# Performance work log

Hardware: AMD Instinct MI355X
Metric: run time of the kernel (lower is better)

The kernel has to match this reference:

```python
import jax, jax.numpy as jnp
import numpy as np

EPS = 1e-6
NUM_HEADS = 16

def layernorm(x, alpha, bias):
    # Faithful to the torch module: torch.std uses ddof=1, and eps is added to std.
    mean = jnp.mean(x, axis=-1, keepdims=True)
    std = jnp.std(x, axis=-1, keepdims=True, ddof=1)
    return alpha * (x - mean) / (std + EPS) + bias

def setup_inputs() -> dict:
    key = jax.random.key(0)
    B, S, D, F = 4, 2048, 1024, 4096
    ks = jax.random.split(key, 8)
    s = 1.0 / np.sqrt(D)
    inp = {
        'x': jax.random.normal(ks[0], (B, S, D), jnp.float32),
        'src_mask': jnp.ones((B, 1, 1, S), jnp.int32),
        'wq': jax.random.normal(ks[1], (D, D), jnp.float32) * s,
        'bq': jnp.zeros((D,), jnp.float32),
        'wk': jax.random.normal(ks[2], (D, D), jnp.float32) * s,
        'bk': jnp.zeros((D,), jnp.float32),
        'wv': jax.random.normal(ks[3], (D, D), jnp.float32) * s,
        'bv': jnp.zeros((D,), jnp.float32),
        'wo': jax.random.normal(ks[4], (D, D), jnp.float32) * s,
        'bo': jnp.zeros((D,), jnp.float32),
        'w1': jax.random.normal(ks[5], (D, F), jnp.float32) * s,
        'b1': jnp.zeros((F,), jnp.float32),
        'w2': jax.random.normal(ks[6], (F, D), jnp.float32) * (1.0 / np.sqrt(F)),
        'b2': jnp.zeros((D,), jnp.float32),
        'ln1_a': jnp.ones((D,), jnp.float32),
        'ln1_b': jnp.zeros((D,), jnp.float32),
        'ln2_a': jnp.ones((D,), jnp.float32),
        'ln2_b': jnp.zeros((D,), jnp.float32),
    }
    return inp

def mha(x, src_mask, wq, bq, wk, bk, wv, bv, wo, bo):
    B, S, D = x.shape
    H = NUM_HEADS
    dk = D // H
    q = (x @ wq + bq).reshape(B, S, H, dk).transpose(0, 2, 1, 3)  # [B,H,S,dk]
    k = (x @ wk + bk).reshape(B, S, H, dk).transpose(0, 2, 1, 3)
    v = (x @ wv + bv).reshape(B, S, H, dk).transpose(0, 2, 1, 3)
    scores = jnp.einsum('bhqd,bhkd->bhqk', q, k) / np.sqrt(dk)  # [B,H,S,S]
    scores = jnp.where(src_mask == 0, -1e9, scores)
    p = jax.nn.softmax(scores, axis=-1)
    ctx = jnp.einsum('bhqk,bhkd->bhqd', p, v)  # [B,H,S,dk]
    ctx = ctx.transpose(0, 2, 1, 3).reshape(B, S, D)
    return ctx @ wo + bo

def reference(x, src_mask, wq, bq, wk, bk, wv, bv, wo, bo,
              w1, b1, w2, b2, ln1_a, ln1_b, ln2_a, ln2_b):
    # residual 1: pre-norm self-attention (dropout is identity in eval)
    h = x + mha(layernorm(x, ln1_a, ln1_b), src_mask, wq, bq, wk, bk, wv, bv, wo, bo)
    # residual 2: pre-norm FFN
    hn = layernorm(h, ln2_a, ln2_b)
    ffn = jax.nn.relu(hn @ w1 + b1) @ w2 + b2
    return h + ffn
```

## Files before the change

kernel.cpp:

```cpp
#include <hip/hip_runtime.h>
#include <hip/hip_bf16.h>

typedef __attribute__((ext_vector_type(8))) short bf16x8;
typedef __attribute__((ext_vector_type(4))) short bf16x4;
typedef __attribute__((ext_vector_type(4))) float f32x4;
typedef __hip_bfloat16 bf16;
typedef unsigned short u16;

#define B_ 4
#define S_ 2048
#define D_ 1024
#define F_ 4096
#define H_ 16
#define MROWS 8192
#define QSCALE 0.18033688011116012f

__device__ __forceinline__ unsigned pkbf(float lo, float hi){
  union{float f; unsigned u;} a, b; a.f = lo; b.f = hi;
  return __builtin_amdgcn_perm(b.u + 0x8000u, a.u + 0x8000u, 0x07060302);
}
__device__ __forceinline__ u16 bfrnd(float f){
  union{float ff; unsigned u;} c; c.ff = f;
  return (u16)((c.u + 0x8000u) >> 16);
}
__device__ __forceinline__ void gll16(const bf16* gp, u16* lp){
  __builtin_amdgcn_global_load_lds(
      (const __attribute__((address_space(1))) void*)gp,
      (__attribute__((address_space(3))) void*)lp, 16, 0, 0);
}

struct PrepArgs { const float* w[6]; const float* b[3]; };
__global__ __launch_bounds__(256) void prep(
    PrepArgs pa, bf16* __restrict__ wqkvoT, bf16* __restrict__ w1T,
    bf16* __restrict__ w2T, float* __restrict__ bqkv)
{
  __shared__ float tl[32][33];
  const int bid = blockIdx.x, tid = threadIdx.x;
  const int x = tid&31, y = tid>>5;
  if (bid < 12288) {
    const float* W; bf16* dst; int K, N, nb, kb;
    if (bid < 4096)      { int wi=bid>>10, t=bid&1023; W=pa.w[wi]; dst=wqkvoT+(size_t)wi*1048576; K=1024; N=1024; nb=t&31;  kb=t>>5; }
    else if (bid < 8192) { int t=bid-4096;             W=pa.w[4];  dst=w1T;  K=1024; N=4096; nb=t&127; kb=t>>7; }
    else                 { int t=bid-8192;             W=pa.w[5];  dst=w2T;  K=4096; N=1024; nb=t&31;  kb=t>>5; }
    const int n0=nb*32, k0=kb*32;
    #pragma unroll
    for (int i=0;i<32;i+=8)
      tl[y+i][x] = W[(size_t)(k0+y+i)*N + n0+x];
    __syncthreads();
    #pragma unroll
    for (int i=0;i<32;i+=8)
      dst[(size_t)(n0+y+i)*K + k0+x] = __float2bfloat16(tl[x][y+i]);
  } else {
    for (int i=tid; i<3072; i+=256) bqkv[i] = pa.b[i>>10][i&1023];
  }
}

__global__ __launch_bounds__(256) void v_transpose(
    const bf16* __restrict__ qkv, bf16* __restrict__ vT)
{
  __shared__ u16 tile[64*65];
  const int bh = blockIdx.y, b = bh>>4, h = bh&15;
  const int s0 = blockIdx.x*64;
  const int tid = threadIdx.x;
  const bf16* src = qkv + (size_t)(b*S_ + s0)*3072 + 2048 + h*64;
  #pragma unroll
  for (int i=0;i<2;i++){
    int idx = i*256 + tid;
    int r = idx>>3, sg = idx&7;
    uint4 v = *reinterpret_cast<const uint4*>(src + (size_t)r*3072 + sg*8);
    const u16* e = (const u16*)&v;
    #pragma unroll
    for (int j=0;j<8;j++) tile[r*65 + sg*8 + j] = e[j];
  }
  __syncthreads();
  bf16* dst = vT + (size_t)bh*64*S_ + s0;
  #pragma unroll
  for (int i=0;i<2;i++){
    int idx = i*256 + tid;
    int d = idx>>3, sg = idx&7;
    u16 tmp[8];
    #pragma unroll
    for (int j=0;j<8;j++) tmp[j] = tile[(sg*8+j)*65 + d];
    *reinterpret_cast<uint4*>(dst + (size_t)d*S_ + sg*8) = *reinterpret_cast<uint4*>(tmp);
  }
}

__device__ __forceinline__ float block_reduce_256(float v, float* sbuf){
  #pragma unroll
  for (int o=32;o>0;o>>=1) v += __shfl_down(v, o);
  int wave = threadIdx.x>>6;
  if ((threadIdx.x&63)==0) sbuf[wave] = v;
  __syncthreads();
  float r = sbuf[0]+sbuf[1]+sbuf[2]+sbuf[3];
  __syncthreads();
  return r;
}

__global__ __launch_bounds__(256) void ln_fwd(
    const float* __restrict__ x, const float* __restrict__ alpha,
    const float* __restrict__ beta, bf16* __restrict__ out)
{
  __shared__ float sbuf[4];
  int row = blockIdx.x, tid = threadIdx.x;
  const float4* xr = reinterpret_cast<const float4*>(x + (size_t)row*D_);
  float4 v = xr[tid];
  float sum = block_reduce_256(v.x+v.y+v.z+v.w, sbuf);
  float mean = sum * (1.0f/1024.0f);
  float dx0=v.x-mean, dx1=v.y-mean, dx2=v.z-mean, dx3=v.w-mean;
  float ssq = block_reduce_256(dx0*dx0+dx1*dx1+dx2*dx2+dx3*dx3, sbuf);
  float std_ = sqrtf(ssq * (1.0f/1023.0f));
  float inv = 1.0f/(std_ + 1e-6f);
  const float4* ar = reinterpret_cast<const float4*>(alpha);
  const float4* br = reinterpret_cast<const float4*>(beta);
  float4 a = ar[tid], bb = br[tid];
  unsigned* o = reinterpret_cast<unsigned*>(out + (size_t)row*D_);
  o[tid*2+0] = pkbf(a.x*dx0*inv + bb.x, a.y*dx1*inv + bb.y);
  o[tid*2+1] = pkbf(a.z*dx2*inv + bb.z, a.w*dx3*inv + bb.w);
}

template<int EPI>
__global__ __launch_bounds__(512) void gemm_bt(
    const bf16* __restrict__ A, const bf16* __restrict__ BT,
    const float* __restrict__ bias, const float* __restrict__ res,
    void* __restrict__ out, int M, int N, int K)
{
  __shared__ __align__(16) u16 As[128*32];
  __shared__ __align__(16) u16 Bs[128*32];
  const int tid = threadIdx.x;
  const int m0 = blockIdx.x*128, n0 = blockIdx.y*128;
  const int wave = tid>>6, lane = tid&63;
  const int wm = (wave>>2)*64, wn = (wave&3)*32;
  const int lrow = lane&15, quad = lane>>4;
  const int srow = wave*16 + (lane>>2);
  const int sseg = lane&3;
  const bf16* apg = A  + (size_t)(m0+srow)*K + sseg*8;
  const bf16* bpg = BT + (size_t)(n0+srow)*K + sseg*8;
  u16* asd = &As[wave*512];
  u16* bsd = &Bs[wave*512];

  f32x4 acc[4][2];
  #pragma unroll
  for (int i=0;i<4;i++)
    #pragma unroll
    for (int j=0;j<2;j++) acc[i][j] = (f32x4){0.f,0.f,0.f,0.f};

  for (int k0=0; k0<K; k0+=32) {
    gll16(apg + k0, asd);
    gll16(bpg + k0, bsd);
    __syncthreads();
    bf16x8 a[4], b[2];
    #pragma unroll
    for (int t=0;t<4;t++)
      a[t] = *reinterpret_cast<const bf16x8*>(&As[(wm + t*16 + lrow)*32 + quad*8]);
    #pragma unroll
    for (int t=0;t<2;t++)
      b[t] = *reinterpret_cast<const bf16x8*>(&Bs[(wn + t*16 + lrow)*32 + quad*8]);
    #pragma unroll
    for (int mt=0;mt<4;mt++)
      #pragma unroll
      for (int nt=0;nt<2;nt++)
        acc[mt][nt] = __builtin_amdgcn_mfma_f32_16x16x32_bf16(a[mt], b[nt], acc[mt][nt], 0,0,0);
    __syncthreads();
  }

  #pragma unroll
  for (int mt=0;mt<4;mt++){
    #pragma unroll
    for (int nt=0;nt<2;nt++){
      int col = n0 + wn + nt*16 + lrow;
      float bv = bias[col];
      float sc = (EPI == 3 && col < 1024) ? QSCALE : 1.0f;
      #pragma unroll
      for (int r=0;r<4;r++){
        int row = m0 + wm + mt*16 + quad*4 + r;
        size_t idx = (size_t)row*N + col;
        float val = acc[mt][nt][r] + bv;
        if (EPI == 1) val = fmaxf(val, 0.0f);
        if (EPI == 3) val *= sc;
        if (EPI == 2) {
          ((float*)out)[idx] = val + res[idx];
        } else {
          ((u16*)out)[idx] = bfrnd(val);
        }
      }
    }
  }
}

#define LA256(bu,hf) (lds + (((bu)*2+0)*2+(hf))*8192)
#define LB256(bu,hf) (lds + (((bu)*2+1)*2+(hf))*8192)

__device__ __forceinline__ bf16x8 ldfrag(const u16* base, int row, int chunk){
  int pc = chunk ^ (row & 7);
  return *reinterpret_cast<const bf16x8*>(base + row*64 + pc*8);
}

__device__ __forceinline__ void stage_half256(const bf16* __restrict__ src, int K,
                                              u16* lbase, int wave, int lane){
  #pragma unroll
  for (int i=0;i<2;i++){
    int q = i*512 + wave*64 + lane;
    int row = q>>3;
    int seg = (q&7) ^ (row&7);
    gll16(src + (size_t)row*K + seg*8, lbase + (i*512 + wave*64)*8);
  }
}

template<int RH, int KS, bool RB, typename STG, typename TAIL>
__device__ __forceinline__ void gphase(const u16* pa, const u16* pb, int bcol,
    int lr, int quad, bf16x8 (&b)[4][2], f32x4 (&acc)[8][4], STG stg, TAIL tail)
{
  bf16x8 a_[4];
  #pragma unroll
  for (int ar=0; ar<4; ar++)
    a_[ar] = ldfrag(pa, RH*64 + ar*16 + lr, KS*4 + quad);
  if constexpr (RB){
    #pragma unroll
    for (int cb=0; cb<4; cb++){
      b[cb][0] = ldfrag(pb, bcol + cb*16 + lr, quad);
      b[cb][1] = ldfrag(pb, bcol + cb*16 + lr, 4 + quad);
    }
  }
  stg();
  __builtin_amdgcn_s_barrier();
  asm volatile("s_waitcnt lgkmcnt(0)" ::: "memory");
  __builtin_amdgcn_sched_barrier(0);
  __builtin_amdgcn_s_setprio(1);
  #pragma unroll
  for (int ar=0; ar<4; ar++)
    #pragma unroll
    for (int cb=0; cb<4; cb++)
      acc[RH*4+ar][cb] = __builtin_amdgcn_mfma_f32_16x16x32_bf16(a_[ar], b[cb][KS], acc[RH*4+ar][cb], 0,0,0);
  __builtin_amdgcn_s_setprio(0);
  tail();
  __builtin_amdgcn_s_barrier();
}

template<int EPI>
__global__ __launch_bounds__(512) void gemm256(
    const bf16* __restrict__ A, const bf16* __restrict__ BT,
    const float* __restrict__ bias, bf16* __restrict__ out, int N, int K)
{
  __shared__ __align__(16) u16 lds[65536];
  const int tid = threadIdx.x, wave = tid>>6, lane = tid&63;
  const int wr = wave>>2, wc = wave&3;
  const int lr = lane&15, quad = lane>>4;
  const int gx = gridDim.x;
  const int nwg = gx*gridDim.y;
  int flat = blockIdx.y*gx + blockIdx.x;
  int cpx = nwg>>3;
  int swz = (flat&7)*cpx + (flat>>3);
  const int m0 = (swz % gx)*256, n0 = (swz / gx)*256;
  const int T = K>>6;

  const bf16* Ag = A  + (size_t)m0*K;
  const bf16* Bg = BT + (size_t)n0*K;
  const int bcol = (wc&1)*64;

  f32x4 acc[8][4];
  #pragma unroll
  for (int i=0;i<8;i++)
    #pragma unroll
    for (int j=0;j<4;j++) acc[i][j] = (f32x4){0.f,0.f,0.f,0.f};

  stage_half256(Ag,                       K, LA256(0,0), wave, lane);
  stage_half256(Ag + (size_t)128*K,       K, LA256(0,1), wave, lane);
  stage_half256(Bg,                       K, LB256(0,0), wave, lane);
  stage_half256(Bg + (size_t)128*K,       K, LB256(0,1), wave, lane);
  stage_half256(Bg + 64,                  K, LB256(1,0), wave, lane);
  stage_half256(Bg + (size_t)128*K + 64,  K, LB256(1,1), wave, lane);
  asm volatile("s_waitcnt vmcnt(4)" ::: "memory");
  __builtin_amdgcn_s_barrier();

  for (int t=0; t<T; ++t){
    const int bu = t&1, nbu = bu^1;
    const u16* pa = LA256(bu, wr);
    const u16* pb = LB256(bu, wc>>1);
    const size_t ktA = (size_t)((t+1 < T) ? t+1 : T-1)*64;
    const size_t ktB = (size_t)((t+2 < T) ? t+2 : T-1)*64;
    bf16x8 b[4][2];
    gphase<0,0,true >(pa, pb, bcol, lr, quad, b, acc,
        [&]{ stage_half256(Ag + ktA,                 K, LA256(nbu,0), wave, lane); }, [&]{});
    gphase<1,0,false>(pa, pb, bcol, lr, quad, b, acc,
        [&]{ stage_half256(Ag + (size_t)128*K + ktA, K, LA256(nbu,1), wave, lane); }, [&]{});
    gphase<0,1,false>(pa, pb, bcol, lr, quad, b, acc,
        [&]{ stage_half256(Bg + ktB,                 K, LB256(bu,0),  wave, lane); }, [&]{});
    gphase<1,1,false>(pa, pb, bcol, lr, quad, b, acc,
        [&]{ stage_half256(Bg + (size_t)128*K + ktB, K, LB256(bu,1),  wave, lane); },
        [&]{ asm volatile("s_waitcnt vmcnt(4)" ::: "memory"); });
  }

  #pragma unroll
  for (int mi=0; mi<8; mi++){
    const int row0 = m0 + wr*128 + (mi>>2)*64 + (mi&3)*16 + quad*4;
    #pragma unroll
    for (int cb=0; cb<4; cb++){
      const int col = n0 + wc*64 + cb*16 + lr;
      float bv = bias[col];
      float sc = (EPI==3 && col < 1024) ? QSCALE : 1.0f;
      #pragma unroll
      for (int r=0; r<4; r++){
        float val = acc[mi][cb][r] + bv;
        if (EPI == 1) val = fmaxf(val, 0.0f);
        if (EPI == 3) val *= sc;
        ((u16*)out)[(size_t)(row0+r)*N + col] = bfrnd(val);
      }
    }
  }
}

#define KP 72

__global__ __launch_bounds__(512) void flash_attn_mfma(
    const bf16* __restrict__ qkv, const bf16* __restrict__ vT,
    const int* __restrict__ mask, bf16* __restrict__ ctx)
{
  __shared__ __align__(16) u16 Ks[64*KP];
  __shared__ __align__(16) u16 Vt[64*64];
  __shared__ __align__(16) float Mb[64];

  const int b = blockIdx.z, h = blockIdx.y, qt = blockIdx.x;
  const int tid = threadIdx.x, wave = tid>>6, lane = tid&63;
  const int lr = lane&15, quad = lane>>4;
  const int qbase = qt*256 + wave*32;

  const bf16* base = qkv + (size_t)b*S_*3072 + h*64;
  const bf16* vtb  = vT + (size_t)(b*H_+h)*64*S_;
  const int*  mrow = mask + b*S_;

  bf16x8 qf[2][2];
  #pragma unroll
  for (int c=0;c<2;c++){
    const bf16* qp = base + (size_t)(qbase + c*16 + lr)*3072 + quad*8;
    qf[c][0] = *reinterpret_cast<const bf16x8*>(qp);
    qf[c][1] = *reinterpret_cast<const bf16x8*>(qp + 32);
  }

  const bf16x4 ones4 = {(short)0x3F80,(short)0x3F80,(short)0x3F80,(short)0x3F80};

  f32x4 actx[2][4];
  f32x4 acc_l[2];
  #pragma unroll
  for (int c=0;c<2;c++){
    #pragma unroll
    for (int dt=0;dt<4;dt++) actx[c][dt] = (f32x4){0.f,0.f,0.f,0.f};
    acc_l[c] = (f32x4){0.f,0.f,0.f,0.f};
  }

  const int sr = tid>>3, sg = tid&7;

  for (int kt=0; kt<S_; kt+=64){
    *reinterpret_cast<uint4*>(&Ks[sr*KP + sg*8]) =
      *reinterpret_cast<const uint4*>(base + 1024 + (size_t)(kt+sr)*3072 + sg*8);
    *reinterpret_cast<uint4*>(&Vt[sr*64 + ((sg ^ (sr&7))<<3)]) =
      *reinterpret_cast<const uint4*>(vtb + (size_t)sr*S_ + kt + sg*8);
    if (tid < 64) Mb[tid] = (mrow[kt+tid]==0) ? -2e9f : 0.0f;
    unsigned long long bal = __ballot(mrow[kt + lane] == 0);
    __syncthreads();

    bf16x4 pk[2][4];
    if (bal == 0ULL) {
      #pragma unroll
      for (int nt=0;nt<4;nt++){
        bf16x8 kf0 = *reinterpret_cast<const bf16x8*>(&Ks[(nt*16+lr)*KP + quad*8]);
        bf16x8 kf1 = *reinterpret_cast<const bf16x8*>(&Ks[(nt*16+lr)*KP + 32 + quad*8]);
        #pragma unroll
        for (int c=0;c<2;c++){
          f32x4 a = (f32x4){0.f,0.f,0.f,0.f};
          a = __builtin_amdgcn_mfma_f32_16x16x32_bf16(kf0, qf[c][0], a, 0,0,0);
          a = __builtin_amdgcn_mfma_f32_16x16x32_bf16(kf1, qf[c][1], a, 0,0,0);
          uint2 w;
          w.x = pkbf(__builtin_amdgcn_exp2f(a[0]), __builtin_amdgcn_exp2f(a[1]));
          w.y = pkbf(__builtin_amdgcn_exp2f(a[2]), __builtin_amdgcn_exp2f(a[3]));
          union{uint2 u; bf16x4 v;} cvt; cvt.u = w;
          pk[c][nt] = cvt.v;
        }
      }
    } else {
      #pragma unroll
      for (int nt=0;nt<4;nt++){
        bf16x8 kf0 = *reinterpret_cast<const bf16x8*>(&Ks[(nt*16+lr)*KP + quad*8]);
        bf16x8 kf1 = *reinterpret_cast<const bf16x8*>(&Ks[(nt*16+lr)*KP + 32 + quad*8]);
        float4 mb = *reinterpret_cast<const float4*>(&Mb[nt*16 + quad*4]);
        #pragma unroll
        for (int c=0;c<2;c++){
          f32x4 a = (f32x4){0.f,0.f,0.f,0.f};
          a = __builtin_amdgcn_mfma_f32_16x16x32_bf16(kf0, qf[c][0], a, 0,0,0);
          a = __builtin_amdgcn_mfma_f32_16x16x32_bf16(kf1, qf[c][1], a, 0,0,0);
          uint2 w;
          w.x = pkbf(__builtin_amdgcn_exp2f(a[0]+mb.x), __builtin_amdgcn_exp2f(a[1]+mb.y));
          w.y = pkbf(__builtin_amdgcn_exp2f(a[2]+mb.z), __builtin_amdgcn_exp2f(a[3]+mb.w));
          union{uint2 u; bf16x4 v;} cvt; cvt.u = w;
          pk[c][nt] = cvt.v;
        }
      }
    }

    #pragma unroll
    for (int dt=0;dt<4;dt++){
      #pragma unroll
      for (int kc=0;kc<4;kc++){
        int voff = ((((kc<<1) + (quad>>1)) ^ (lr&7))<<3) + ((quad&1)<<2);
        bf16x4 vf = *reinterpret_cast<const bf16x4*>(&Vt[(dt*16+lr)*64 + voff]);
        #pragma unroll
        for (int c=0;c<2;c++)
          actx[c][dt] = __builtin_amdgcn_mfma_f32_16x16x16bf16_1k(vf, pk[c][kc], actx[c][dt], 0,0,0);
      }
    }
    #pragma unroll
    for (int kc=0;kc<4;kc++)
      #pragma unroll
      for (int c=0;c<2;c++)
        acc_l[c] = __builtin_amdgcn_mfma_f32_16x16x16bf16_1k(ones4, pk[c][kc], acc_l[c], 0,0,0);
    __syncthreads();
  }

  #pragma unroll
  for (int c=0;c<2;c++){
    float inv = 1.0f/acc_l[c][0];
    int q = qbase + c*16 + lr;
    bf16* op = ctx + (size_t)(b*S_+q)*D_ + h*64 + quad*4;
    #pragma unroll
    for (int dt=0;dt<4;dt++){
      uint2 o;
      o.x = pkbf(actx[c][dt][0]*inv, actx[c][dt][1]*inv);
      o.y = pkbf(actx[c][dt][2]*inv, actx[c][dt][3]*inv);
      *reinterpret_cast<uint2*>(op + dt*16) = o;
    }
  }
}

extern "C" void kernel_launch(void* const* d_in, const int* in_sizes, int n_in,
                              void* d_out, int out_size, void* d_ws, size_t ws_size,
                              hipStream_t stream) {
  const float* x    = (const float*)d_in[0];
  const int*   mask = (const int*)  d_in[1];
  const float* wq   = (const float*)d_in[2];
  const float* bq   = (const float*)d_in[3];
  const float* wk   = (const float*)d_in[4];
  const float* bk   = (const float*)d_in[5];
  const float* wv   = (const float*)d_in[6];
  const float* bv   = (const float*)d_in[7];
  const float* wo   = (const float*)d_in[8];
  const float* bo   = (const float*)d_in[9];
  const float* w1   = (const float*)d_in[10];
  const float* b1   = (const float*)d_in[11];
  const float* w2   = (const float*)d_in[12];
  const float* b2   = (const float*)d_in[13];
  const float* ln1a = (const float*)d_in[14];
  const float* ln1b = (const float*)d_in[15];
  const float* ln2a = (const float*)d_in[16];
  const float* ln2b = (const float*)d_in[17];

  char* ws = (char*)d_ws;
  bf16*  wqkvT = (bf16*) (ws + 0);
  bf16*  woT   = (bf16*) (ws + 6291456);
  bf16*  w1T   = (bf16*) (ws + 8388608);
  bf16*  w2T   = (bf16*) (ws + 16777216);
  float* bqkv  = (float*)(ws + 25165824);
  bf16*  xn    = (bf16*) (ws + 25178112);
  bf16*  vT    = (bf16*) (ws + 25178112);
  bf16*  qkv   = (bf16*) (ws + 41955328);
  bf16*  ctx   = (bf16*) (ws + 92286976);
  bf16*  hn    = (bf16*) (ws + 109064192);
  bf16*  act   = (bf16*) (ws + 25178112);

  PrepArgs pa;
  pa.w[0]=wq; pa.w[1]=wk; pa.w[2]=wv; pa.w[3]=wo; pa.w[4]=w1; pa.w[5]=w2;
  pa.b[0]=bq; pa.b[1]=bk; pa.b[2]=bv;
  prep<<<12289,256,0,stream>>>(pa, wqkvT, w1T, w2T, bqkv);

  ln_fwd<<<8192,256,0,stream>>>(x, ln1a, ln1b, xn);
  gemm256<3><<<dim3(32,12),512,0,stream>>>(xn, wqkvT, bqkv, qkv, 3072, 1024);
  v_transpose<<<dim3(32,64),256,0,stream>>>(qkv, vT);
  flash_attn_mfma<<<dim3(S_/256,H_,B_),512,0,stream>>>(qkv, vT, mask, ctx);
  gemm_bt<2><<<dim3(64,8),512,0,stream>>>(ctx, woT, bo, x, d_out, MROWS,1024,1024);
  ln_fwd<<<8192,256,0,stream>>>((const float*)d_out, ln2a, ln2b, hn);
  gemm256<1><<<dim3(32,16),512,0,stream>>>(hn, w1T, b1, act, F_, 1024);
  gemm_bt<2><<<dim3(64,8),512,0,stream>>>(act, w2T, b2, (const float*)d_out, d_out, MROWS,1024,F_);
}
```

Before: 527.1 us.

## Add pipelined 256x128 residual GEMM and pad attention V tile in LDS

Result: no change. 526.4 us (-0.1%).

```diff
diff --git a/kernel.cpp b/kernel.cpp
--- a/kernel.cpp
+++ b/kernel.cpp
@@ -309,6 +309,106 @@
   }
 }
 
+#define LA2(bu,hf) (lds2 + ((bu)*3+(hf))*8192)
+#define LB2(bu)    (lds2 + ((bu)*3+2)*8192)
+
+template<int RH, int KS, bool RB, typename STG, typename TAIL>
+__device__ __forceinline__ void gphase2(const u16* pa, const u16* pb, int bcol,
+    int lr, int quad, bf16x8 (&b)[2][2], f32x4 (&acc)[8][2], STG stg, TAIL tail)
+{
+  bf16x8 a_[4];
+  #pragma unroll
+  for (int ar=0; ar<4; ar++)
+    a_[ar] = ldfrag(pa, RH*64 + ar*16 + lr, KS*4 + quad);
+  if constexpr (RB){
+    #pragma unroll
+    for (int cb=0; cb<2; cb++){
+      b[cb][0] = ldfrag(pb, bcol + cb*16 + lr, quad);
+      b[cb][1] = ldfrag(pb, bcol + cb*16 + lr, 4 + quad);
+    }
+  }
+  stg();
+  __builtin_amdgcn_s_barrier();
+  asm volatile("s_waitcnt lgkmcnt(0)" ::: "memory");
+  __builtin_amdgcn_sched_barrier(0);
+  __builtin_amdgcn_s_setprio(1);
+  #pragma unroll
+  for (int ar=0; ar<4; ar++)
+    #pragma unroll
+    for (int cb=0; cb<2; cb++)
+      acc[RH*4+ar][cb] = __builtin_amdgcn_mfma_f32_16x16x32_bf16(a_[ar], b[cb][KS], acc[RH*4+ar][cb], 0,0,0);
+  __builtin_amdgcn_s_setprio(0);
+  tail();
+  __builtin_amdgcn_s_barrier();
+}
+
+__global__ __launch_bounds__(512) void gemm256r(
+    const bf16* __restrict__ A, const bf16* __restrict__ BT,
+    const float* __restrict__ bias, const float* __restrict__ res,
+    float* __restrict__ out, int N, int K)
+{
+  __shared__ __align__(16) u16 lds2[49152];
+  const int tid = threadIdx.x, wave = tid>>6, lane = tid&63;
+  const int wr = wave>>2, wc = wave&3;
+  const int lr = lane&15, quad = lane>>4;
+  const int gx = gridDim.x;
+  const int nwg = gx*gridDim.y;
+  int flat = blockIdx.y*gx + blockIdx.x;
+  int cpx = nwg>>3;
+  int swz = (flat&7)*cpx + (flat>>3);
+  const int m0 = (swz % gx)*256, n0 = (swz / gx)*128;
+  const int T = K>>6;
+
+  const bf16* Ag = A  + (size_t)m0*K;
+  const bf16* Bg = BT + (size_t)n0*K;
+  const int bcol = wc*32;
+
+  f32x4 acc[8][2];
+  #pragma unroll
+  for (int i=0;i<8;i++)
+    #pragma unroll
+    for (int j=0;j<2;j++) acc[i][j] = (f32x4){0.f,0.f,0.f,0.f};
+
+  stage_half256(Ag,                 K, LA2(0,0), wave, lane);
+  stage_half256(Ag + (size_t)128*K, K, LA2(0,1), wave, lane);
+  stage_half256(Bg,                 K, LB2(0),   wave, lane);
+  stage_half256(Bg + 64,            K, LB2(1),   wave, lane);
+  asm volatile("s_waitcnt vmcnt(2)" ::: "memory");
+  __builtin_amdgcn_s_barrier();
+
+  for (int t=0; t<T; ++t){
+    const int bu = t&1, nbu = bu^1;
+    const u16* pa = LA2(bu, wr);
+    const u16* pb = LB2(bu);
+    const size_t ktA = (size_t)((t+1 < T) ? t+1 : T-1)*64;
+    const size_t ktB = (size_t)((t+2 < T) ? t+2 : T-1)*64;
+    bf16x8 b[2][2];
+    gphase2<0,0,true >(pa, pb, bcol, lr, quad, b, acc,
+        [&]{ stage_half256(Ag + ktA,                 K, LA2(nbu,0), wave, lane); }, [&]{});
+    gphase2<1,0,false>(pa, pb, bcol, lr, quad, b, acc,
+        [&]{ stage_half256(Ag + (size_t)128*K + ktA, K, LA2(nbu,1), wave, lane); }, [&]{});
+    gphase2<0,1,false>(pa, pb, bcol, lr, quad, b, acc,
+        [&]{ stage_half256(Bg + ktB,                 K, LB2(bu),    wave, lane); }, [&]{});
+    gphase2<1,1,false>(pa, pb, bcol, lr, quad, b, acc,
+        [&]{}, [&]{ asm volatile("s_waitcnt vmcnt(2)" ::: "memory"); });
+  }
+
+  #pragma unroll
+  for (int mi=0; mi<8; mi++){
+    const int row0 = m0 + wr*128 + (mi>>2)*64 + (mi&3)*16 + quad*4;
+    #pragma unroll
+    for (int cb=0; cb<2; cb++){
+      const int col = n0 + bcol + cb*16 + lr;
+      float bv = bias[col];
+      #pragma unroll
+      for (int r=0; r<4; r++){
+        size_t idx = (size_t)(row0+r)*N + col;
+        out[idx] = acc[mi][cb][r] + bv + res[idx];
+      }
+    }
+  }
+}
+
 #define KP 72
 
 __global__ __launch_bounds__(512) void flash_attn_mfma(
@@ -316,7 +416,7 @@
     const int* __restrict__ mask, bf16* __restrict__ ctx)
 {
   __shared__ __align__(16) u16 Ks[64*KP];
-  __shared__ __align__(16) u16 Vt[64*64];
+  __shared__ __align__(16) u16 Vt[64*KP];
   __shared__ __align__(16) float Mb[64];
 
   const int b = blockIdx.z, h = blockIdx.y, qt = blockIdx.x;
@@ -352,7 +452,7 @@
   for (int kt=0; kt<S_; kt+=64){
     *reinterpret_cast<uint4*>(&Ks[sr*KP + sg*8]) =
       *reinterpret_cast<const uint4*>(base + 1024 + (size_t)(kt+sr)*3072 + sg*8);
-    *reinterpret_cast<uint4*>(&Vt[sr*64 + ((sg ^ (sr&7))<<3)]) =
+    *reinterpret_cast<uint4*>(&Vt[sr*KP + sg*8]) =
       *reinterpret_cast<const uint4*>(vtb + (size_t)sr*S_ + kt + sg*8);
     if (tid < 64) Mb[tid] = (mrow[kt+tid]==0) ? -2e9f : 0.0f;
     unsigned long long bal = __ballot(mrow[kt + lane] == 0);
@@ -400,8 +500,7 @@
     for (int dt=0;dt<4;dt++){
       #pragma unroll
       for (int kc=0;kc<4;kc++){
-        int voff = ((((kc<<1) + (quad>>1)) ^ (lr&7))<<3) + ((quad&1)<<2);
-        bf16x4 vf = *reinterpret_cast<const bf16x4*>(&Vt[(dt*16+lr)*64 + voff]);
+        bf16x4 vf = *reinterpret_cast<const bf16x4*>(&Vt[(dt*16+lr)*KP + kc*16 + quad*4]);
         #pragma unroll
         for (int c=0;c<2;c++)
           actx[c][dt] = __builtin_amdgcn_mfma_f32_16x16x16bf16_1k(vf, pk[c][kc], actx[c][dt], 0,0,0);
@@ -474,8 +573,8 @@
   gemm256<3><<<dim3(32,12),512,0,stream>>>(xn, wqkvT, bqkv, qkv, 3072, 1024);
   v_transpose<<<dim3(32,64),256,0,stream>>>(qkv, vT);
   flash_attn_mfma<<<dim3(S_/256,H_,B_),512,0,stream>>>(qkv, vT, mask, ctx);
-  gemm_bt<2><<<dim3(64,8),512,0,stream>>>(ctx, woT, bo, x, d_out, MROWS,1024,1024);
+  gemm256r<<<dim3(32,8),512,0,stream>>>(ctx, woT, bo, x, (float*)d_out, 1024, 1024);
   ln_fwd<<<8192,256,0,stream>>>((const float*)d_out, ln2a, ln2b, hn);
   gemm256<1><<<dim3(32,16),512,0,stream>>>(hn, w1T, b1, act, F_, 1024);
-  gemm_bt<2><<<dim3(64,8),512,0,stream>>>(act, w2T, b2, (const float*)d_out, d_out, MROWS,1024,F_);
-}
+  gemm256r<<<dim3(32,8),512,0,stream>>>(act, w2T, b2, (const float*)d_out, (float*)d_out, 1024, 4096);
+}
```
